# Performance work log

Hardware: AMD Instinct MI355X
Metric: run time of the kernel (lower is better)

The kernel has to match this reference:

```python
import jax, jax.numpy as jnp
import numpy as np

C = 256      # channels
H = 8        # num_heads
D = C // H   # head_dim = 32
K = 128      # patch_size
N = 100000   # number of points
M = 131072   # total path tokens (4 segments of 32768, each multiple of K)


def setup_inputs() -> dict:
    key = jax.random.key(0)
    ks = jax.random.split(key, 8)
    feat = jax.random.normal(ks[0], (N, C), dtype=jnp.float32)
    path_coord = jax.random.normal(ks[1], (M, 3), dtype=jnp.float32)
    path_inverse = jax.random.randint(ks[2], (M,), 0, N, dtype=jnp.int32)
    # 4 segments, each length 32768 (multiple of K) -> pad/unpad are identity
    path_offset = jnp.array([32768, 65536, 98304, 131072], dtype=jnp.int32)
    # RoPE tables: position within each K-block, NeoX-style, last dim = head_dim
    half = D // 2
    pos = (jnp.arange(M) % K).astype(jnp.float32)
    inv_freq = 1.0 / (10000.0 ** (jnp.arange(half, dtype=jnp.float32) / half))
    freqs = pos[:, None] * inv_freq[None, :]                 # [M, D/2]
    cos = jnp.concatenate([jnp.cos(freqs), jnp.cos(freqs)], axis=-1)  # [M, D]
    sin = jnp.concatenate([jnp.sin(freqs), jnp.sin(freqs)], axis=-1)
    Wqkv = jax.random.normal(ks[3], (3 * C, C), dtype=jnp.float32) * 0.02
    bqkv = jnp.zeros((3 * C,), dtype=jnp.float32)
    Wproj = jax.random.normal(ks[4], (C, C), dtype=jnp.float32) * 0.02
    bproj = jnp.zeros((C,), dtype=jnp.float32)
    return {"feat": feat, "path_coord": path_coord, "path_inverse": path_inverse,
            "path_offset": path_offset, "cos": cos, "sin": sin,
            "Wqkv": Wqkv, "bqkv": bqkv, "Wproj": Wproj, "bproj": bproj}


def _rope(t, c, s):
    # NeoX half-split rotation; t: [M, H, D], c/s: [M, 1, D/2]
    t1, t2 = t[..., : D // 2], t[..., D // 2:]
    return jnp.concatenate([t1 * c - t2 * s, t2 * c + t1 * s], axis=-1)


def reference(feat, path_coord, path_inverse, path_offset, cos, sin,
              Wqkv, bqkv, Wproj, bproj):
    scale = D ** -0.5
    # qkv projection then gather to path tokens (pad is identity here)
    qkv = feat @ Wqkv.T + bqkv                    # [N, 3C]
    x = qkv[path_inverse].reshape(M, 3, H, D)     # [M, 3, H, D]
    q, k, v = x[:, 0], x[:, 1], x[:, 2]
    c = cos[:, : D // 2][:, None, :]              # [M, 1, D/2]
    s = sin[:, : D // 2][:, None, :]
    q = _rope(q, c, s)
    k = _rope(k, c, s)
    # block attention within fixed K-token patches (flash_attn_varlen equivalent)
    P = M // K
    qb = q.reshape(P, K, H, D)
    kb = k.reshape(P, K, H, D)
    vb = v.reshape(P, K, H, D)
    scores = jnp.einsum("pqhd,pkhd->phqk", qb, kb) * scale
    attn = jax.nn.softmax(scores, axis=-1)
    out = jnp.einsum("phqk,pkhd->pqhd", attn, vb).reshape(M, C)
    out = out @ Wproj.T + bproj                   # [M, C]
    # scatter-mean back to points over path_inverse
    sums = jax.ops.segment_sum(out, path_inverse, num_segments=N)
    cnt = jax.ops.segment_sum(jnp.ones((M, 1), out.dtype), path_inverse,
                              num_segments=N)
    return jnp.where(cnt > 0, sums / jnp.maximum(cnt, 1.0), 0.0)
```

## Files before the change

### kernel.cpp

```cpp
#include <hip/hip_runtime.h>
#include <stdint.h>

#define N_PTS 100000
#define M_PTS 131072

typedef unsigned short u16;
typedef __attribute__((ext_vector_type(8))) short bf16x8;
typedef __attribute__((ext_vector_type(4))) float f32x4;

__device__ __forceinline__ u16 f2bf(float x) {
    union { float f; uint32_t u; } v; v.f = x;
    uint32_t r = v.u + 0x7fffu + ((v.u >> 16) & 1u);
    return (u16)(r >> 16);
}
__device__ __forceinline__ float bf2f(u16 b) {
    union { uint32_t u; float f; } v; v.u = ((uint32_t)b) << 16;
    return v.f;
}
__device__ __forceinline__ bf16x8 cvt8(const float* __restrict__ p) {
    float4 x0 = *(const float4*)p;
    float4 x1 = *(const float4*)(p + 4);
    bf16x8 r;
    r[0]=(short)f2bf(x0.x); r[1]=(short)f2bf(x0.y);
    r[2]=(short)f2bf(x0.z); r[3]=(short)f2bf(x0.w);
    r[4]=(short)f2bf(x1.x); r[5]=(short)f2bf(x1.y);
    r[6]=(short)f2bf(x1.z); r[7]=(short)f2bf(x1.w);
    return r;
}

__global__ __launch_bounds__(256) void conv_weights(
    const float* __restrict__ Wqkv, const float* __restrict__ Wproj,
    u16* __restrict__ Wqkvb, u16* __restrict__ Wprojb)
{
    int i = blockIdx.x*256 + threadIdx.x;
    Wqkvb[i] = f2bf(Wqkv[i]);
    if (i < 65536) Wprojb[i] = f2bf(Wproj[i]);
}

__global__ __launch_bounds__(512) void qkv_gemm(
    const float* __restrict__ feat, const u16* __restrict__ Wqkvb,
    const float* __restrict__ bqkv, u16* __restrict__ qkvb)
{
    const int nt = blockIdx.x;
    const int tid = threadIdx.x;
    __shared__ u16 at[128][256];

    {
        const int row = tid >> 2, q = tid & 3;
        const int grow = nt*128 + row;
        const int swb = row & 7;
        if (grow < N_PTS) {
            const float* src = feat + (size_t)grow*256;
            #pragma unroll
            for (int i=0;i<8;i++) {
                int c = i*4 + q;
                bf16x8 v = cvt8(src + c*8);
                *(bf16x8*)&at[row][(c^swb)*8] = v;
            }
        } else {
            #pragma unroll
            for (int i=0;i<8;i++) {
                int c = i*4 + q;
                *(bf16x8*)&at[row][(c^swb)*8] = (bf16x8)0;
            }
        }
    }
    __syncthreads();

    const int w = tid>>6, l = tid&63, lr = l&15, lk = l>>4;
    const int r0 = (w>>2)*64;
    const int n0 = nt*128 + r0;
    const int swr = lr & 7;

    for (int jt=0; jt<3; jt++) {
        const int j0 = jt*256 + (w&3)*64;
        f32x4 acc[4][4];
        #pragma unroll
        for (int a=0;a<4;a++)
          #pragma unroll
          for (int b=0;b<4;b++) acc[a][b] = (f32x4)0.0f;

        for (int k=0;k<256;k+=32) {
            const int cc = (k>>3) + lk;
            bf16x8 af[4], bfr[4];
            #pragma unroll
            for (int f=0;f<4;f++)
                af[f] = *(const bf16x8*)&at[r0 + f*16 + lr][(cc^swr)*8];
            #pragma unroll
            for (int f=0;f<4;f++)
                bfr[f] = *(const bf16x8*)(Wqkvb + (size_t)(j0 + f*16 + lr)*256 + k + lk*8);
            #pragma unroll
            for (int a=0;a<4;a++)
              #pragma unroll
              for (int b=0;b<4;b++)
                acc[a][b] = __builtin_amdgcn_mfma_f32_16x16x32_bf16(af[a], bfr[b], acc[a][b], 0,0,0);
        }
        #pragma unroll
        for (int a=0;a<4;a++) {
          #pragma unroll
          for (int b=0;b<4;b++) {
            int col = j0 + b*16 + lr;
            float bias = bqkv[col];
            #pragma unroll
            for (int r=0;r<4;r++) {
                int row = n0 + a*16 + lk*4 + r;
                if (row < N_PTS)
                    qkvb[(size_t)row*768 + col] = f2bf(acc[a][b][r] + bias);
            }
          }
        }
    }
}

__global__ __launch_bounds__(256) void attn_kernel(
    const u16* __restrict__ qkvb, const int* __restrict__ pinv,
    const float* __restrict__ cosb, const float* __restrict__ sinb,
    u16* __restrict__ attnout)
{
    const int h = blockIdx.x;
    const int p = blockIdx.y;
    const int tid = threadIdx.x;

    __shared__ u16 qb[128][40];
    __shared__ u16 kb[128][40];
    __shared__ u16 vT[32][136];
    __shared__ u16 Pb[128][136];

    {
        const int i = tid >> 1, part = tid & 1;
        const int m = p*128 + i;
        const int r = pinv[m];
        const u16* base = qkvb + (size_t)r*768 + part*256 + h*32;
        u16 vals[32];
        *(uint4*)(vals+0)  = *(const uint4*)(base+0);
        *(uint4*)(vals+8)  = *(const uint4*)(base+8);
        *(uint4*)(vals+16) = *(const uint4*)(base+16);
        *(uint4*)(vals+24) = *(const uint4*)(base+24);
        const float* cr = cosb + (size_t)m*32;
        const float* sr = sinb + (size_t)m*32;
        u16 o[32];
        #pragma unroll
        for (int d=0; d<16; d++) {
            float x1 = bf2f(vals[d]), x2 = bf2f(vals[d+16]);
            float c = cr[d], s = sr[d];
            o[d]    = f2bf(x1*c - x2*s);
            o[d+16] = f2bf(x2*c + x1*s);
        }
        u16 (*dst)[40] = part ? kb : qb;
        *(uint4*)&dst[i][0]  = *(uint4*)(o+0);
        *(uint4*)&dst[i][8]  = *(uint4*)(o+8);
        *(uint4*)&dst[i][16] = *(uint4*)(o+16);
        *(uint4*)&dst[i][24] = *(uint4*)(o+24);
        if (part) {
            const u16* vbase = qkvb + (size_t)r*768 + 512 + h*32;
            #pragma unroll
            for (int dd=0; dd<32; dd+=8) {
                u16 tv[8];
                *(uint4*)tv = *(const uint4*)(vbase+dd);
                #pragma unroll
                for (int b=0;b<8;b++) vT[dd+b][i] = tv[b];
            }
        }
    }
    __syncthreads();

    const int w = tid>>6, l = tid&63, lr = l&15, lk = l>>4;
    const float scale = 0.17677669529663687f;

    f32x4 sf[2][8];
    #pragma unroll
    for (int mt=0; mt<2; mt++) {
        const int rb = w*32 + mt*16;
        bf16x8 a = *(const bf16x8*)&qb[rb+lr][lk*8];
        #pragma unroll
        for (int nt=0; nt<8; nt++) {
            bf16x8 b = *(const bf16x8*)&kb[nt*16+lr][lk*8];
            sf[mt][nt] = __builtin_amdgcn_mfma_f32_16x16x32_bf16(a, b, (f32x4)0.0f, 0,0,0);
        }
    }
    #pragma unroll
    for (int mt=0; mt<2; mt++) {
      #pragma unroll
      for (int r=0; r<4; r++) {
        float mx = -1e30f;
        #pragma unroll
        for (int nt=0; nt<8; nt++) {
            sf[mt][nt][r] *= scale;
            mx = fmaxf(mx, sf[mt][nt][r]);
        }
        #pragma unroll
        for (int msk=1; msk<16; msk<<=1) mx = fmaxf(mx, __shfl_xor(mx, msk));
        float sum = 0.f;
        #pragma unroll
        for (int nt=0; nt<8; nt++) {
            float e = __expf(sf[mt][nt][r] - mx);
            sf[mt][nt][r] = e;
            sum += e;
        }
        #pragma unroll
        for (int msk=1; msk<16; msk<<=1) sum += __shfl_xor(sum, msk);
        float inv = 1.f / sum;
        int row = w*32 + mt*16 + lk*4 + r;
        #pragma unroll
        for (int nt=0; nt<8; nt++)
            Pb[row][nt*16+lr] = f2bf(sf[mt][nt][r] * inv);
      }
    }
    #pragma unroll
    for (int mt=0; mt<2; mt++) {
        const int rb = w*32 + mt*16;
        #pragma unroll
        for (int nt=0; nt<2; nt++) {
            f32x4 acc = (f32x4)0.0f;
            #pragma unroll
            for (int ks=0; ks<4; ks++) {
                bf16x8 a = *(const bf16x8*)&Pb[rb+lr][ks*32 + lk*8];
                bf16x8 b = *(const bf16x8*)&vT[nt*16+lr][ks*32 + lk*8];
                acc = __builtin_amdgcn_mfma_f32_16x16x32_bf16(a, b, acc, 0,0,0);
            }
            #pragma unroll
            for (int r=0;r<4;r++) {
                int token = p*128 + rb + lk*4 + r;
                attnout[(size_t)token*256 + h*32 + nt*16 + lr] = f2bf(acc[r]);
            }
        }
    }
}

__global__ __launch_bounds__(256) void fill_kernel(const int* __restrict__ pinv,
                                                   int* __restrict__ cursor,
                                                   int* __restrict__ list)
{
    int m = blockIdx.x*256 + threadIdx.x;
    if (m < M_PTS) {
        int seg = pinv[m];
        int slot = atomicAdd(cursor + seg, 1);
        if (slot < 32) list[seg*32 + slot] = m;
    }
}

__global__ __launch_bounds__(256) void seg_mean(
    const u16* __restrict__ attnout, const int* __restrict__ cursor,
    const int* __restrict__ list, u16* __restrict__ meanb)
{
    int idx = blockIdx.x*256 + threadIdx.x;
    int seg = idx >> 3, c8 = idx & 7;
    if (seg >= N_PTS) return;
    int c = cursor[seg];
    int cc = c < 32 ? c : 32;
    float acc[32];
    #pragma unroll
    for (int j=0;j<32;j++) acc[j] = 0.f;
    const int* lp = list + seg*32;
    for (int i=0;i<cc;i++) {
        int m = lp[i];
        const u16* src = attnout + (size_t)m*256 + c8*32;
        #pragma unroll
        for (int ch=0;ch<4;ch++) {
            bf16x8 v = *(const bf16x8*)(src + ch*8);
            #pragma unroll
            for (int j=0;j<8;j++) acc[ch*8+j] += bf2f((u16)v[j]);
        }
    }
    float inv = (c > 0) ? 1.f/(float)c : 0.f;
    u16* dst = meanb + (size_t)seg*256 + c8*32;
    #pragma unroll
    for (int ch=0;ch<4;ch++) {
        bf16x8 o;
        #pragma unroll
        for (int j=0;j<8;j++) o[j] = (short)f2bf(acc[ch*8+j]*inv);
        *(bf16x8*)(dst + ch*8) = o;
    }
}

__global__ __launch_bounds__(512) void mean_proj(
    const u16* __restrict__ meanb, const int* __restrict__ cursor,
    const u16* __restrict__ Wprojb, const float* __restrict__ bproj,
    float* __restrict__ out)
{
    const int nt = blockIdx.x;
    const int tid = threadIdx.x;
    __shared__ u16 at[128][256];

    {
        const int row = tid >> 2, q = tid & 3;
        const int grow = nt*128 + row;
        const int swb = row & 7;
        if (grow < N_PTS) {
            const u16* src = meanb + (size_t)grow*256;
            #pragma unroll
            for (int i=0;i<8;i++) {
                int cix = i*4 + q;
                bf16x8 v = *(const bf16x8*)(src + cix*8);
                *(bf16x8*)&at[row][(cix^swb)*8] = v;
            }
        } else {
            #pragma unroll
            for (int i=0;i<8;i++) {
                int cix = i*4 + q;
                *(bf16x8*)&at[row][(cix^swb)*8] = (bf16x8)0;
            }
        }
    }
    __syncthreads();

    const int w = tid>>6, l = tid&63, lr = l&15, lk = l>>4;
    const int r0 = (w>>2)*64;
    const int n0 = nt*128 + r0;
    const int j0 = (w&3)*64;
    const int swr = lr & 7;

    f32x4 acc[4][4];
    #pragma unroll
    for (int a=0;a<4;a++)
      #pragma unroll
      for (int b=0;b<4;b++) acc[a][b] = (f32x4)0.0f;

    for (int k=0;k<256;k+=32) {
        const int cc = (k>>3) + lk;
        bf16x8 af[4], bfr[4];
        #pragma unroll
        for (int f=0;f<4;f++)
            af[f] = *(const bf16x8*)&at[r0 + f*16 + lr][(cc^swr)*8];
        #pragma unroll
        for (int f=0;f<4;f++)
            bfr[f] = *(const bf16x8*)(Wprojb + (size_t)(j0 + f*16 + lr)*256 + k + lk*8);
        #pragma unroll
        for (int a=0;a<4;a++)
          #pragma unroll
          for (int b=0;b<4;b++)
            acc[a][b] = __builtin_amdgcn_mfma_f32_16x16x32_bf16(af[a], bfr[b], acc[a][b], 0,0,0);
    }
    #pragma unroll
    for (int a=0;a<4;a++) {
      #pragma unroll
      for (int b=0;b<4;b++) {
        int col = j0 + b*16 + lr;
        float bias = bproj[col];
        #pragma unroll
        for (int r=0;r<4;r++) {
            int row = n0 + a*16 + lk*4 + r;
            if (row < N_PTS) {
                int c = cursor[row];
                out[(size_t)row*256 + col] = (c > 0) ? acc[a][b][r] + bias : 0.f;
            }
        }
      }
    }
}

extern "C" void kernel_launch(void* const* d_in, const int* in_sizes, int n_in,
                              void* d_out, int out_size, void* d_ws, size_t ws_size,
                              hipStream_t stream)
{
    const float* feat  = (const float*)d_in[0];
    const int*   pinv  = (const int*)d_in[2];
    const float* cosb  = (const float*)d_in[4];
    const float* sinb  = (const float*)d_in[5];
    const float* Wqkv  = (const float*)d_in[6];
    const float* bqkv  = (const float*)d_in[7];
    const float* Wproj = (const float*)d_in[8];
    const float* bproj = (const float*)d_in[9];
    float* out = (float*)d_out;

    char* ws = (char*)d_ws;
    u16* qkvb = (u16*)ws;
    u16* meanb = (u16*)ws;
    int* list  = (int*)(ws + 70000000);
    int* cursor= (int*)(ws + 90000000);
    size_t off0 = (size_t)N_PTS*768*2;
    u16* attnout = (u16*)(ws + off0);
    size_t off2 = off0 + (size_t)M_PTS*256*2;
    u16* Wqkvb = (u16*)(ws + off2);
    size_t off3 = off2 + (size_t)768*256*2;
    u16* Wprojb = (u16*)(ws + off3);

    conv_weights <<<768, 256, 0, stream>>>(Wqkv, Wproj, Wqkvb, Wprojb);
    qkv_gemm     <<<782, 512, 0, stream>>>(feat, Wqkvb, bqkv, qkvb);
    attn_kernel  <<<dim3(8, 1024), 256, 0, stream>>>(qkvb, pinv, cosb, sinb, attnout);
    hipMemsetAsync(cursor, 0, (size_t)N_PTS*sizeof(int), stream);
    fill_kernel  <<<512, 256, 0, stream>>>(pinv, cursor, list);
    seg_mean     <<<3125, 256, 0, stream>>>(attnout, cursor, list, meanb);
    mean_proj    <<<782, 512, 0, stream>>>(meanb, cursor, Wprojb, bproj, out);
}
```

Baseline: 595.0 us.

## Halve GEMM row tiles and interleave QKV per head for contiguous attention gathers

Both GEMM kernels now use 64-row tiles instead of 128, with each of the 8 waves covering 32 output columns across all 64 rows. This doubles the grid and halves LDS per block, aiming for better occupancy and load balance across CUs. The QKV output layout is also changed to head-interleaved [h][q|k|v][d], so each attention gather reads one contiguous 192-byte span per head instead of three scattered 64-byte chunks. The trade-off is more redundant weight reads per output and less register reuse per MFMA.

```diff
diff --git a/kernel.cpp b/kernel.cpp
--- a/kernel.cpp
+++ b/kernel.cpp
@@ -43,24 +43,24 @@
 {
     const int nt = blockIdx.x;
     const int tid = threadIdx.x;
-    __shared__ u16 at[128][256];
+    __shared__ u16 at[64][256];
 
     {
-        const int row = tid >> 2, q = tid & 3;
-        const int grow = nt*128 + row;
+        const int row = tid >> 3, q = tid & 7;
+        const int grow = nt*64 + row;
         const int swb = row & 7;
         if (grow < N_PTS) {
             const float* src = feat + (size_t)grow*256;
             #pragma unroll
-            for (int i=0;i<8;i++) {
-                int c = i*4 + q;
+            for (int i=0;i<4;i++) {
+                int c = q + i*8;
                 bf16x8 v = cvt8(src + c*8);
                 *(bf16x8*)&at[row][(c^swb)*8] = v;
             }
         } else {
             #pragma unroll
-            for (int i=0;i<8;i++) {
-                int c = i*4 + q;
+            for (int i=0;i<4;i++) {
+                int c = q + i*8;
                 *(bf16x8*)&at[row][(c^swb)*8] = (bf16x8)0;
             }
         }
@@ -68,44 +68,45 @@
     __syncthreads();
 
     const int w = tid>>6, l = tid&63, lr = l&15, lk = l>>4;
-    const int r0 = (w>>2)*64;
-    const int n0 = nt*128 + r0;
+    const int n0 = nt*64;
     const int swr = lr & 7;
 
     for (int jt=0; jt<3; jt++) {
-        const int j0 = jt*256 + (w&3)*64;
-        f32x4 acc[4][4];
+        const int j0 = jt*256 + w*32;
+        f32x4 acc[4][2];
         #pragma unroll
         for (int a=0;a<4;a++)
           #pragma unroll
-          for (int b=0;b<4;b++) acc[a][b] = (f32x4)0.0f;
+          for (int b=0;b<2;b++) acc[a][b] = (f32x4)0.0f;
 
         for (int k=0;k<256;k+=32) {
             const int cc = (k>>3) + lk;
-            bf16x8 af[4], bfr[4];
+            bf16x8 af[4], bfr[2];
+            #pragma unroll
+            for (int b=0;b<2;b++)
+                bfr[b] = *(const bf16x8*)(Wqkvb + (size_t)(j0 + b*16 + lr)*256 + k + lk*8);
             #pragma unroll
             for (int f=0;f<4;f++)
-                af[f] = *(const bf16x8*)&at[r0 + f*16 + lr][(cc^swr)*8];
-            #pragma unroll
-            for (int f=0;f<4;f++)
-                bfr[f] = *(const bf16x8*)(Wqkvb + (size_t)(j0 + f*16 + lr)*256 + k + lk*8);
+                af[f] = *(const bf16x8*)&at[f*16 + lr][(cc^swr)*8];
             #pragma unroll
             for (int a=0;a<4;a++)
               #pragma unroll
-              for (int b=0;b<4;b++)
+              for (int b=0;b<2;b++)
                 acc[a][b] = __builtin_amdgcn_mfma_f32_16x16x32_bf16(af[a], bfr[b], acc[a][b], 0,0,0);
         }
         #pragma unroll
         for (int a=0;a<4;a++) {
           #pragma unroll
-          for (int b=0;b<4;b++) {
+          for (int b=0;b<2;b++) {
             int col = j0 + b*16 + lr;
             float bias = bqkv[col];
+            int part = col >> 8, hh = (col >> 5) & 7, d = col & 31;
+            size_t cofs = (size_t)hh*96 + part*32 + d;
             #pragma unroll
             for (int r=0;r<4;r++) {
                 int row = n0 + a*16 + lk*4 + r;
                 if (row < N_PTS)
-                    qkvb[(size_t)row*768 + col] = f2bf(acc[a][b][r] + bias);
+                    qkvb[(size_t)row*768 + cofs] = f2bf(acc[a][b][r] + bias);
             }
           }
         }
@@ -130,7 +131,7 @@
         const int i = tid >> 1, part = tid & 1;
         const int m = p*128 + i;
         const int r = pinv[m];
-        const u16* base = qkvb + (size_t)r*768 + part*256 + h*32;
+        const u16* base = qkvb + (size_t)r*768 + h*96 + part*32;
         u16 vals[32];
         *(uint4*)(vals+0)  = *(const uint4*)(base+0);
         *(uint4*)(vals+8)  = *(const uint4*)(base+8);
@@ -152,7 +153,7 @@
         *(uint4*)&dst[i][16] = *(uint4*)(o+16);
         *(uint4*)&dst[i][24] = *(uint4*)(o+24);
         if (part) {
-            const u16* vbase = qkvb + (size_t)r*768 + 512 + h*32;
+            const u16* vbase = base + 32;
             #pragma unroll
             for (int dd=0; dd<32; dd+=8) {
                 u16 tv[8];
@@ -280,61 +281,60 @@
 {
     const int nt = blockIdx.x;
     const int tid = threadIdx.x;
-    __shared__ u16 at[128][256];
+    __shared__ u16 at[64][256];
 
     {
-        const int row = tid >> 2, q = tid & 3;
-        const int grow = nt*128 + row;
+        const int row = tid >> 3, q = tid & 7;
+        const int grow = nt*64 + row;
         const int swb = row & 7;
         if (grow < N_PTS) {
             const u16* src = meanb + (size_t)grow*256;
             #pragma unroll
-            for (int i=0;i<8;i++) {
-                int cix = i*4 + q;
-                bf16x8 v = *(const bf16x8*)(src + cix*8);
-                *(bf16x8*)&at[row][(cix^swb)*8] = v;
+            for (int i=0;i<4;i++) {
+                int c = q + i*8;
+                bf16x8 v = *(const bf16x8*)(src + c*8);
+                *(bf16x8*)&at[row][(c^swb)*8] = v;
             }
         } else {
             #pragma unroll
-            for (int i=0;i<8;i++) {
-                int cix = i*4 + q;
-                *(bf16x8*)&at[row][(cix^swb)*8] = (bf16x8)0;
+            for (int i=0;i<4;i++) {
+                int c = q + i*8;
+                *(bf16x8*)&at[row][(c^swb)*8] = (bf16x8)0;
             }
         }
     }
     __syncthreads();
 
     const int w = tid>>6, l = tid&63, lr = l&15, lk = l>>4;
-    const int r0 = (w>>2)*64;
-    const int n0 = nt*128 + r0;
-    const int j0 = (w&3)*64;
+    const int n0 = nt*64;
+    const int j0 = w*32;
     const int swr = lr & 7;
 
-    f32x4 acc[4][4];
+    f32x4 acc[4][2];
     #pragma unroll
     for (int a=0;a<4;a++)
       #pragma unroll
-      for (int b=0;b<4;b++) acc[a][b] = (f32x4)0.0f;
+      for (int b=0;b<2;b++) acc[a][b] = (f32x4)0.0f;
 
     for (int k=0;k<256;k+=32) {
         const int cc = (k>>3) + lk;
-        bf16x8 af[4], bfr[4];
+        bf16x8 af[4], bfr[2];
+        #pragma unroll
+        for (int b=0;b<2;b++)
+            bfr[b] = *(const bf16x8*)(Wprojb + (size_t)(j0 + b*16 + lr)*256 + k + lk*8);
         #pragma unroll
         for (int f=0;f<4;f++)
-            af[f] = *(const bf16x8*)&at[r0 + f*16 + lr][(cc^swr)*8];
-        #pragma unroll
-        for (int f=0;f<4;f++)
-            bfr[f] = *(const bf16x8*)(Wprojb + (size_t)(j0 + f*16 + lr)*256 + k + lk*8);
+            af[f] = *(const bf16x8*)&at[f*16 + lr][(cc^swr)*8];
         #pragma unroll
         for (int a=0;a<4;a++)
           #pragma unroll
-          for (int b=0;b<4;b++)
+          for (int b=0;b<2;b++)
             acc[a][b] = __builtin_amdgcn_mfma_f32_16x16x32_bf16(af[a], bfr[b], acc[a][b], 0,0,0);
     }
     #pragma unroll
     for (int a=0;a<4;a++) {
       #pragma unroll
-      for (int b=0;b<4;b++) {
+      for (int b=0;b<2;b++) {
         int col = j0 + b*16 + lr;
         float bias = bproj[col];
         #pragma unroll
@@ -376,10 +376,10 @@
     u16* Wprojb = (u16*)(ws + off3);
 
     conv_weights <<<768, 256, 0, stream>>>(Wqkv, Wproj, Wqkvb, Wprojb);
-    qkv_gemm     <<<782, 512, 0, stream>>>(feat, Wqkvb, bqkv, qkvb);
+    qkv_gemm     <<<1563, 512, 0, stream>>>(feat, Wqkvb, bqkv, qkvb);
     attn_kernel  <<<dim3(8, 1024), 256, 0, stream>>>(qkvb, pinv, cosb, sinb, attnout);
     hipMemsetAsync(cursor, 0, (size_t)N_PTS*sizeof(int), stream);
     fill_kernel  <<<512, 256, 0, stream>>>(pinv, cursor, list);
     seg_mean     <<<3125, 256, 0, stream>>>(attnout, cursor, list, meanb);
-    mean_proj    <<<782, 512, 0, stream>>>(meanb, cursor, Wprojb, bproj, out);
-}
+    mean_proj    <<<1563, 512, 0, stream>>>(meanb, cursor, Wprojb, bproj, out);
+}
```

Result: faster. 571.2 us (-4.0%).

## Double-buffer both GEMMs with direct-to-LDS loads and interleave QKV per head

Applied to the files above, without the earlier changes.

Adds a single pre-pass that converts feat and both weight matrices to bf16. Both projection GEMMs are rewritten as 128x128 output tiles that stage A and B through double-buffered LDS using global_load_lds, replacing the old design of a full 128x256 A tile plus B fragments read straight from global memory. The QKV output is stored head-interleaved (q, k, v for one head side by side), so the attention gather reads one contiguous span per token. The trade-offs are an extra bf16 copy of feat written to workspace and more blocks, each with a barrier per k-step.

```diff
diff --git a/kernel.cpp b/kernel.cpp
--- a/kernel.cpp
+++ b/kernel.cpp
@@ -27,88 +27,92 @@
     r[6]=(short)f2bf(x1.z); r[7]=(short)f2bf(x1.w);
     return r;
 }
-
-__global__ __launch_bounds__(256) void conv_weights(
-    const float* __restrict__ Wqkv, const float* __restrict__ Wproj,
-    u16* __restrict__ Wqkvb, u16* __restrict__ Wprojb)
-{
-    int i = blockIdx.x*256 + threadIdx.x;
-    Wqkvb[i] = f2bf(Wqkv[i]);
-    if (i < 65536) Wprojb[i] = f2bf(Wproj[i]);
-}
-
-__global__ __launch_bounds__(512) void qkv_gemm(
-    const float* __restrict__ feat, const u16* __restrict__ Wqkvb,
+__device__ __forceinline__ void gload_lds16(const u16* g, u16* l) {
+    __builtin_amdgcn_global_load_lds(
+        (const __attribute__((address_space(1))) void*)g,
+        (__attribute__((address_space(3))) void*)l, 16, 0, 0);
+}
+
+__global__ __launch_bounds__(256) void conv_all(
+    const float* __restrict__ feat, const float* __restrict__ Wqkv,
+    const float* __restrict__ Wproj,
+    u16* __restrict__ featb, u16* __restrict__ Wqkvb, u16* __restrict__ Wprojb)
+{
+    int gid = blockIdx.x*256 + threadIdx.x;
+    for (int c = gid; c < 3200000; c += 2048*256)
+        *(bf16x8*)(featb + (size_t)c*8) = cvt8(feat + (size_t)c*8);
+    if (gid < 24576) *(bf16x8*)(Wqkvb + (size_t)gid*8) = cvt8(Wqkv + (size_t)gid*8);
+    if (gid < 8192)  *(bf16x8*)(Wprojb + (size_t)gid*8) = cvt8(Wproj + (size_t)gid*8);
+}
+
+__global__ __launch_bounds__(256, 4) void qkv_gemm(
+    const u16* __restrict__ featb, const u16* __restrict__ Wqkvb,
     const float* __restrict__ bqkv, u16* __restrict__ qkvb)
 {
-    const int nt = blockIdx.x;
+    const int jt = blockIdx.x;
+    const int nt = blockIdx.y;
     const int tid = threadIdx.x;
-    __shared__ u16 at[128][256];
-
-    {
-        const int row = tid >> 2, q = tid & 3;
-        const int grow = nt*128 + row;
-        const int swb = row & 7;
-        if (grow < N_PTS) {
-            const float* src = feat + (size_t)grow*256;
-            #pragma unroll
-            for (int i=0;i<8;i++) {
-                int c = i*4 + q;
-                bf16x8 v = cvt8(src + c*8);
-                *(bf16x8*)&at[row][(c^swb)*8] = v;
-            }
-        } else {
-            #pragma unroll
-            for (int i=0;i<8;i++) {
-                int c = i*4 + q;
-                *(bf16x8*)&at[row][(c^swb)*8] = (bf16x8)0;
-            }
-        }
-    }
+    __shared__ u16 As[2][128*32];
+    __shared__ u16 Bs[2][128*32];
+
+    const int n0 = nt*128, j0 = jt*128;
+    const int srow = tid >> 2, schk = (tid & 3) * 8;
+    const u16* aS = featb + (size_t)(n0 + srow)*256 + schk;
+    const u16* bS = Wqkvb + (size_t)(j0 + srow)*256 + schk;
+
+#define STAGE_QKV(buf, k0) do { \
+    gload_lds16(aS + (k0),                   &As[buf][tid*8]); \
+    gload_lds16(aS + (size_t)64*256 + (k0),  &As[buf][2048 + tid*8]); \
+    gload_lds16(bS + (k0),                   &Bs[buf][tid*8]); \
+    gload_lds16(bS + (size_t)64*256 + (k0),  &Bs[buf][2048 + tid*8]); \
+  } while (0)
+
+    STAGE_QKV(0, 0);
     __syncthreads();
 
     const int w = tid>>6, l = tid&63, lr = l&15, lk = l>>4;
-    const int r0 = (w>>2)*64;
-    const int n0 = nt*128 + r0;
-    const int swr = lr & 7;
-
-    for (int jt=0; jt<3; jt++) {
-        const int j0 = jt*256 + (w&3)*64;
-        f32x4 acc[4][4];
+    const int r0 = (w>>1)*64, c0 = (w&1)*64;
+
+    f32x4 acc[4][4];
+    #pragma unroll
+    for (int a=0;a<4;a++)
+      #pragma unroll
+      for (int b=0;b<4;b++) acc[a][b] = (f32x4)0.0f;
+
+    for (int t=0; t<8; ++t) {
+        const int buf = t & 1;
+        if (t < 7) STAGE_QKV(buf^1, (t+1)*32);
+        bf16x8 af[4], bfr[4];
+        #pragma unroll
+        for (int f=0;f<4;f++)
+            af[f]  = *(const bf16x8*)&As[buf][(r0 + f*16 + lr)*32 + lk*8];
+        #pragma unroll
+        for (int f=0;f<4;f++)
+            bfr[f] = *(const bf16x8*)&Bs[buf][(c0 + f*16 + lr)*32 + lk*8];
         #pragma unroll
         for (int a=0;a<4;a++)
           #pragma unroll
-          for (int b=0;b<4;b++) acc[a][b] = (f32x4)0.0f;
-
-        for (int k=0;k<256;k+=32) {
-            const int cc = (k>>3) + lk;
-            bf16x8 af[4], bfr[4];
-            #pragma unroll
-            for (int f=0;f<4;f++)
-                af[f] = *(const bf16x8*)&at[r0 + f*16 + lr][(cc^swr)*8];
-            #pragma unroll
-            for (int f=0;f<4;f++)
-                bfr[f] = *(const bf16x8*)(Wqkvb + (size_t)(j0 + f*16 + lr)*256 + k + lk*8);
-            #pragma unroll
-            for (int a=0;a<4;a++)
-              #pragma unroll
-              for (int b=0;b<4;b++)
-                acc[a][b] = __builtin_amdgcn_mfma_f32_16x16x32_bf16(af[a], bfr[b], acc[a][b], 0,0,0);
-        }
-        #pragma unroll
-        for (int a=0;a<4;a++) {
-          #pragma unroll
-          for (int b=0;b<4;b++) {
-            int col = j0 + b*16 + lr;
-            float bias = bqkv[col];
-            #pragma unroll
-            for (int r=0;r<4;r++) {
-                int row = n0 + a*16 + lk*4 + r;
-                if (row < N_PTS)
-                    qkvb[(size_t)row*768 + col] = f2bf(acc[a][b][r] + bias);
-            }
-          }
-        }
+          for (int b=0;b<4;b++)
+            acc[a][b] = __builtin_amdgcn_mfma_f32_16x16x32_bf16(af[a], bfr[b], acc[a][b], 0,0,0);
+        __syncthreads();
+    }
+#undef STAGE_QKV
+
+    #pragma unroll
+    for (int a=0;a<4;a++) {
+      #pragma unroll
+      for (int b=0;b<4;b++) {
+        int col = j0 + c0 + b*16 + lr;
+        float bias = bqkv[col];
+        int part = col >> 8, hh = (col >> 5) & 7, d = col & 31;
+        size_t cofs = (size_t)hh*96 + part*32 + d;
+        #pragma unroll
+        for (int r=0;r<4;r++) {
+            int row = n0 + r0 + a*16 + lk*4 + r;
+            if (row < N_PTS)
+                qkvb[(size_t)row*768 + cofs] = f2bf(acc[a][b][r] + bias);
+        }
+      }
     }
 }
 
@@ -130,7 +134,7 @@
         const int i = tid >> 1, part = tid & 1;
         const int m = p*128 + i;
         const int r = pinv[m];
-        const u16* base = qkvb + (size_t)r*768 + part*256 + h*32;
+        const u16* base = qkvb + (size_t)r*768 + h*96 + part*32;
         u16 vals[32];
         *(uint4*)(vals+0)  = *(const uint4*)(base+0);
         *(uint4*)(vals+8)  = *(const uint4*)(base+8);
@@ -152,7 +156,7 @@
         *(uint4*)&dst[i][16] = *(uint4*)(o+16);
         *(uint4*)&dst[i][24] = *(uint4*)(o+24);
         if (part) {
-            const u16* vbase = qkvb + (size_t)r*768 + 512 + h*32;
+            const u16* vbase = base + 32;
             #pragma unroll
             for (int dd=0; dd<32; dd+=8) {
                 u16 tv[8];
@@ -273,42 +277,34 @@
     }
 }
 
-__global__ __launch_bounds__(512) void mean_proj(
+__global__ __launch_bounds__(256, 4) void mean_proj(
     const u16* __restrict__ meanb, const int* __restrict__ cursor,
     const u16* __restrict__ Wprojb, const float* __restrict__ bproj,
     float* __restrict__ out)
 {
-    const int nt = blockIdx.x;
+    const int jt = blockIdx.x;
+    const int nt = blockIdx.y;
     const int tid = threadIdx.x;
-    __shared__ u16 at[128][256];
-
-    {
-        const int row = tid >> 2, q = tid & 3;
-        const int grow = nt*128 + row;
-        const int swb = row & 7;
-        if (grow < N_PTS) {
-            const u16* src = meanb + (size_t)grow*256;
-            #pragma unroll
-            for (int i=0;i<8;i++) {
-                int cix = i*4 + q;
-                bf16x8 v = *(const bf16x8*)(src + cix*8);
-                *(bf16x8*)&at[row][(cix^swb)*8] = v;
-            }
-        } else {
-            #pragma unroll
-            for (int i=0;i<8;i++) {
-                int cix = i*4 + q;
-                *(bf16x8*)&at[row][(cix^swb)*8] = (bf16x8)0;
-            }
-        }
-    }
+    __shared__ u16 As[2][128*32];
+    __shared__ u16 Bs[2][128*32];
+
+    const int n0 = nt*128, j0 = jt*128;
+    const int srow = tid >> 2, schk = (tid & 3) * 8;
+    const u16* aS = meanb  + (size_t)(n0 + srow)*256 + schk;
+    const u16* bS = Wprojb + (size_t)(j0 + srow)*256 + schk;
+
+#define STAGE_MP(buf, k0) do { \
+    gload_lds16(aS + (k0),                   &As[buf][tid*8]); \
+    gload_lds16(aS + (size_t)64*256 + (k0),  &As[buf][2048 + tid*8]); \
+    gload_lds16(bS + (k0),                   &Bs[buf][tid*8]); \
+    gload_lds16(bS + (size_t)64*256 + (k0),  &Bs[buf][2048 + tid*8]); \
+  } while (0)
+
+    STAGE_MP(0, 0);
     __syncthreads();
 
     const int w = tid>>6, l = tid&63, lr = l&15, lk = l>>4;
-    const int r0 = (w>>2)*64;
-    const int n0 = nt*128 + r0;
-    const int j0 = (w&3)*64;
-    const int swr = lr & 7;
+    const int r0 = (w>>1)*64, c0 = (w&1)*64;
 
     f32x4 acc[4][4];
     #pragma unroll
@@ -316,30 +312,34 @@
       #pragma unroll
       for (int b=0;b<4;b++) acc[a][b] = (f32x4)0.0f;
 
-    for (int k=0;k<256;k+=32) {
-        const int cc = (k>>3) + lk;
+    for (int t=0; t<8; ++t) {
+        const int buf = t & 1;
+        if (t < 7) STAGE_MP(buf^1, (t+1)*32);
         bf16x8 af[4], bfr[4];
         #pragma unroll
         for (int f=0;f<4;f++)
-            af[f] = *(const bf16x8*)&at[r0 + f*16 + lr][(cc^swr)*8];
+            af[f]  = *(const bf16x8*)&As[buf][(r0 + f*16 + lr)*32 + lk*8];
         #pragma unroll
         for (int f=0;f<4;f++)
-            bfr[f] = *(const bf16x8*)(Wprojb + (size_t)(j0 + f*16 + lr)*256 + k + lk*8);
+            bfr[f] = *(const bf16x8*)&Bs[buf][(c0 + f*16 + lr)*32 + lk*8];
         #pragma unroll
         for (int a=0;a<4;a++)
           #pragma unroll
           for (int b=0;b<4;b++)
             acc[a][b] = __builtin_amdgcn_mfma_f32_16x16x32_bf16(af[a], bfr[b], acc[a][b], 0,0,0);
-    }
+        __syncthreads();
+    }
+#undef STAGE_MP
+
     #pragma unroll
     for (int a=0;a<4;a++) {
       #pragma unroll
       for (int b=0;b<4;b++) {
-        int col = j0 + b*16 + lr;
+        int col = j0 + c0 + b*16 + lr;
         float bias = bproj[col];
         #pragma unroll
         for (int r=0;r<4;r++) {
-            int row = n0 + a*16 + lk*4 + r;
+            int row = n0 + r0 + a*16 + lk*4 + r;
             if (row < N_PTS) {
                 int c = cursor[row];
                 out[(size_t)row*256 + col] = (c > 0) ? acc[a][b][r] + bias : 0.f;
@@ -370,16 +370,17 @@
     int* cursor= (int*)(ws + 90000000);
     size_t off0 = (size_t)N_PTS*768*2;
     u16* attnout = (u16*)(ws + off0);
+    u16* featb   = (u16*)(ws + off0);
     size_t off2 = off0 + (size_t)M_PTS*256*2;
     u16* Wqkvb = (u16*)(ws + off2);
     size_t off3 = off2 + (size_t)768*256*2;
     u16* Wprojb = (u16*)(ws + off3);
 
-    conv_weights <<<768, 256, 0, stream>>>(Wqkv, Wproj, Wqkvb, Wprojb);
-    qkv_gemm     <<<782, 512, 0, stream>>>(feat, Wqkvb, bqkv, qkvb);
+    conv_all     <<<2048, 256, 0, stream>>>(feat, Wqkv, Wproj, featb, Wqkvb, Wprojb);
+    qkv_gemm     <<<dim3(6, 782), 256, 0, stream>>>(featb, Wqkvb, bqkv, qkvb);
     attn_kernel  <<<dim3(8, 1024), 256, 0, stream>>>(qkvb, pinv, cosb, sinb, attnout);
     hipMemsetAsync(cursor, 0, (size_t)N_PTS*sizeof(int), stream);
     fill_kernel  <<<512, 256, 0, stream>>>(pinv, cursor, list);
     seg_mean     <<<3125, 256, 0, stream>>>(attnout, cursor, list, meanb);
-    mean_proj    <<<782, 512, 0, stream>>>(meanb, cursor, Wprojb, bproj, out);
-}
+    mean_proj    <<<dim3(2, 782), 256, 0, stream>>>(meanb, cursor, Wprojb, bproj, out);
+}
```

New measurement: 517.3 us. 1.15x faster.
